# Kernel tuning notes

Measured on AMD Instinct MI355X. Metric: run time of the kernel, lower is better.

Reference implementation:

```python
import jax, jax.numpy as jnp
import numpy as np

MAX_BIN = 256
N_SAMPLES = 2_000_000
N_FEATURES = 64


def setup_inputs() -> dict:
    key = jax.random.key(0)
    k1, k2, k3 = jax.random.split(key, 3)
    X = jax.random.randint(k1, (N_SAMPLES, N_FEATURES), 0, MAX_BIN, dtype=jnp.int32)
    gradient = jax.random.normal(k2, (N_SAMPLES,), dtype=jnp.float32)
    hessian = jax.random.uniform(k3, (N_SAMPLES,), dtype=jnp.float32)
    return {"X": X, "gradient": gradient, "hessian": hessian}


def reference(X, gradient, hessian):
    # PGBM split_decision: Gl[f, b] = sum_i gradient[i] * (X[i, f] <= b)
    # Implemented as a per-feature histogram scatter-add, then cumsum over bins.
    def per_feature(xf):  # xf: [N] int bins for one feature
        hg = jax.ops.segment_sum(gradient, xf, num_segments=MAX_BIN)
        hh = jax.ops.segment_sum(hessian, xf, num_segments=MAX_BIN)
        return hg, hh

    hist_g, hist_h = jax.vmap(per_feature, in_axes=1)(X)  # [F, MAX_BIN] each
    Gl = jnp.cumsum(hist_g, axis=1)  # left gradient sums per (feature, bin)
    Hl = jnp.cumsum(hist_h, axis=1)  # left hessian sums per (feature, bin)
    return Gl[None], Hl[None]  # [1, F, MAX_BIN] each, matching unsqueeze(0)
```

## Files before the change

kernel.cpp:

```cpp
#include <hip/hip_runtime.h>

#define N_FEAT 64
#define NBINS 256
#define NB2 260
#define HIST_FLOATS (N_FEAT * NBINS)
#define NBLOCKS 256
#define BLOCK_T 128
#define CHUNK 32
#define PARTIAL_FLOATS 32768
#define WS_PARTIAL_BYTES ((size_t)NBLOCKS * PARTIAL_FLOATS * sizeof(float))

__device__ __forceinline__ void load_chunk(const int* __restrict__ X,
    const float* __restrict__ grad, const float* __restrict__ hess,
    int c, int rend, int col, int lane, int (&bins)[CHUNK], float& val)
{
    #pragma unroll
    for (int j = 0; j < CHUNK; ++j) {
        int r = c + j; r = r < rend ? r : rend - 1;
        bins[j] = X[(size_t)r * N_FEAT + col];
    }
    int rv = c + (lane & 31); rv = rv < rend ? rv : rend - 1;
    val = (lane < 32) ? grad[rv] : hess[rv];
}

__device__ __forceinline__ void process_chunk(float (&hist)[2][N_FEAT][NB2],
    int w, int lane, int c, int rend, const int (&bins)[CHUNK], float val)
{
    #pragma unroll
    for (int q = 0; q < CHUNK / 4; ++q) {
        float v[4]; int b[4];
        #pragma unroll
        for (int j = 0; j < 4; ++j) {
            const int r = c + q * 4 + j;
            const float vv = __shfl(val, (lane & 32) + q * 4 + j);
            v[j] = (r < rend) ? vv : 0.f;
            b[j] = bins[q * 4 + j];
        }
        const bool e10 = b[1] == b[0];
        const bool e20 = b[2] == b[0], e21 = b[2] == b[1];
        const bool e30 = b[3] == b[0], e31 = b[3] == b[1], e32 = b[3] == b[2];
        const float v0 = v[0] + (e10 ? v[1] : 0.f) + (e20 ? v[2] : 0.f) + (e30 ? v[3] : 0.f);
        const float v1 = v[1] + ((!e20 && e21) ? v[2] : 0.f) + ((!e30 && e31) ? v[3] : 0.f);
        const float v2 = v[2] + ((!e30 && !e31 && e32) ? v[3] : 0.f);
        const float v3 = v[3];
        const int a0 = b[0];
        const int a1 = e10                 ? 256 : b[1];
        const int a2 = (e20 || e21)        ? 257 : b[2];
        const int a3 = (e30 || e31 || e32) ? 258 : b[3];
        const float t0 = hist[w][lane][a0];
        const float t1 = hist[w][lane][a1];
        const float t2 = hist[w][lane][a2];
        const float t3 = hist[w][lane][a3];
        hist[w][lane][a0] = t0 + v0;
        hist[w][lane][a1] = t1 + v1;
        hist[w][lane][a2] = t2 + v2;
        hist[w][lane][a3] = t3 + v3;
    }
}

__global__ __launch_bounds__(BLOCK_T, 1) void _split_hist_kernel(
    const int* __restrict__ X, const float* __restrict__ grad,
    const float* __restrict__ hess, float* __restrict__ ws, int n, int mode)
{
    __shared__ float hist[2][N_FEAT][NB2];
    const int tid  = threadIdx.x;
    const int w    = tid >> 6;
    const int lane = tid & 63;

    for (int i = tid; i < 2 * N_FEAT * NB2; i += BLOCK_T)
        (&hist[0][0][0])[i] = 0.f;
    __syncthreads();

    const int col  = w * 32 + (lane & 31);
    const int R    = (n + NBLOCKS - 1) / NBLOCKS;
    const int rbeg = blockIdx.x * R;
    const int rend = min(rbeg + R, n);

    if (rbeg < rend) {
        int   binsA[CHUNK], binsB[CHUNK];
        float valA, valB;
        load_chunk(X, grad, hess, rbeg, rend, col, lane, binsA, valA);
        for (int c = rbeg; c < rend; c += 2 * CHUNK) {
            const int c1 = c + CHUNK, c2 = c + 2 * CHUNK;
            if (c1 < rend)
                load_chunk(X, grad, hess, c1, rend, col, lane, binsB, valB);
            process_chunk(hist, w, lane, c, rend, binsA, valA);
            if (c1 < rend) {
                if (c2 < rend)
                    load_chunk(X, grad, hess, c2, rend, col, lane, binsA, valA);
                process_chunk(hist, w, lane, c1, rend, binsB, valB);
            }
        }
    }
    __syncthreads();

    if (mode) {
        float* dst = ws + (size_t)blockIdx.x * PARTIAL_FLOATS;
        for (int i = tid; i < PARTIAL_FLOATS; i += BLOCK_T) {
            const int wv  = i >> 14;
            const int reg = (i >> 8) & 63;
            const int bin = i & 255;
            dst[i] = hist[wv][reg][bin];
        }
    } else {
        for (int i = tid; i < PARTIAL_FLOATS; i += BLOCK_T) {
            const int wv   = i >> 14;
            const int reg  = (i >> 8) & 63;
            const int bin  = i & 255;
            const int type = reg >> 5;
            const int feat = wv * 32 + (reg & 31);
            unsafeAtomicAdd(&ws[type * HIST_FLOATS + feat * NBINS + bin],
                            hist[wv][reg][bin]);
        }
    }
}

__global__ __launch_bounds__(NBINS) void _split_scan_kernel(
    const float* __restrict__ ws, float* __restrict__ out, int mode)
{
    __shared__ float s[NBINS];
    const int row = blockIdx.x;
    const int t   = threadIdx.x;

    float acc;
    if (mode) {
        const int type = row >> 6;
        const int feat = row & 63;
        const int wv   = feat >> 5;
        const int reg  = (type << 5) | (feat & 31);
        const size_t slot = ((size_t)wv << 14) | (reg << 8) | t;
        acc = 0.f;
        for (int p = 0; p < NBLOCKS; ++p)
            acc += ws[(size_t)p * PARTIAL_FLOATS + slot];
    } else {
        acc = ws[row * NBINS + t];
    }
    s[t] = acc;
    __syncthreads();

    #pragma unroll
    for (int off = 1; off < NBINS; off <<= 1) {
        float x = (t >= off) ? s[t - off] : 0.f;
        __syncthreads();
        s[t] += x;
        __syncthreads();
    }
    out[row * NBINS + t] = s[t];
}

extern "C" void kernel_launch(void* const* d_in, const int* in_sizes, int n_in,
                              void* d_out, int out_size, void* d_ws, size_t ws_size,
                              hipStream_t stream) {
    const int*   X    = (const int*)d_in[0];
    const float* grad = (const float*)d_in[1];
    const float* hess = (const float*)d_in[2];
    float*       out  = (float*)d_out;
    float*       ws   = (float*)d_ws;
    const int n = in_sizes[1];

    const int mode = (ws_size >= WS_PARTIAL_BYTES) ? 1 : 0;
    if (!mode)
        hipMemsetAsync(d_ws, 0, 2 * HIST_FLOATS * sizeof(float), stream);

    hipLaunchKernelGGL(_split_hist_kernel, dim3(NBLOCKS), dim3(BLOCK_T), 0, stream,
                       X, grad, hess, ws, n, mode);
    hipLaunchKernelGGL(_split_scan_kernel, dim3(2 * N_FEAT), dim3(NBINS), 0, stream,
                       ws, out, mode);
}
```

Baseline: 1.148 ms.

## Assign one wave per value type with one lane per feature, vectorizing value loads

Each wave now handles either gradient or hessian across all 64 features: each lane owns one feature column, and wave 0 reads gradient while wave 1 reads hessian. Previously each wave covered 32 features and split its lanes between the two value types. Values are now loaded per thread as float4 vectors instead of being broadcast with cross-lane shuffles. Each row's X loads are therefore 64 contiguous ints per wave, and both waves read the same X rows, doubling X read traffic through cache. Rows per block are rounded to a multiple of the chunk size so the fast unguarded load path is taken, and the partial-histogram layout now matches the output directly, simplifying the atomic and scan indexing.

After: 942.9 us. 1.22x faster.

```diff
diff --git a/kernel.cpp b/kernel.cpp
--- a/kernel.cpp
+++ b/kernel.cpp
@@ -7,54 +7,64 @@
 #define NBLOCKS 256
 #define BLOCK_T 128
 #define CHUNK 32
-#define PARTIAL_FLOATS 32768
+#define PARTIAL_FLOATS (2 * HIST_FLOATS)
 #define WS_PARTIAL_BYTES ((size_t)NBLOCKS * PARTIAL_FLOATS * sizeof(float))
 
-__device__ __forceinline__ void load_chunk(const int* __restrict__ X,
-    const float* __restrict__ grad, const float* __restrict__ hess,
-    int c, int rend, int col, int lane, int (&bins)[CHUNK], float& val)
+__device__ __forceinline__ void load_bins(const int* __restrict__ Xl,
+    int c, int rend, int (&bins)[CHUNK])
 {
-    #pragma unroll
-    for (int j = 0; j < CHUNK; ++j) {
-        int r = c + j; r = r < rend ? r : rend - 1;
-        bins[j] = X[(size_t)r * N_FEAT + col];
+    if (c + CHUNK <= rend) {
+        #pragma unroll
+        for (int j = 0; j < CHUNK; ++j)
+            bins[j] = Xl[(size_t)(c + j) * N_FEAT];
+    } else {
+        #pragma unroll
+        for (int j = 0; j < CHUNK; ++j) {
+            int r = c + j; r = r < rend ? r : rend - 1;
+            bins[j] = Xl[(size_t)r * N_FEAT];
+        }
     }
-    int rv = c + (lane & 31); rv = rv < rend ? rv : rend - 1;
-    val = (lane < 32) ? grad[rv] : hess[rv];
 }
 
-__device__ __forceinline__ void process_chunk(float (&hist)[2][N_FEAT][NB2],
-    int w, int lane, int c, int rend, const int (&bins)[CHUNK], float val)
+__device__ __forceinline__ void load_vals(const float* __restrict__ vp,
+    int c, int rend, float (&val)[CHUNK])
+{
+    if (c + CHUNK <= rend) {
+        #pragma unroll
+        for (int j = 0; j < CHUNK / 4; ++j) {
+            const float4 v4 = *reinterpret_cast<const float4*>(vp + c + 4 * j);
+            val[4*j+0] = v4.x; val[4*j+1] = v4.y; val[4*j+2] = v4.z; val[4*j+3] = v4.w;
+        }
+    } else {
+        #pragma unroll
+        for (int j = 0; j < CHUNK; ++j)
+            val[j] = (c + j < rend) ? vp[c + j] : 0.f;
+    }
+}
+
+__device__ __forceinline__ void process_chunk(float* __restrict__ hrow,
+    const int (&bins)[CHUNK], const float (&val)[CHUNK])
 {
     #pragma unroll
     for (int q = 0; q < CHUNK / 4; ++q) {
-        float v[4]; int b[4];
-        #pragma unroll
-        for (int j = 0; j < 4; ++j) {
-            const int r = c + q * 4 + j;
-            const float vv = __shfl(val, (lane & 32) + q * 4 + j);
-            v[j] = (r < rend) ? vv : 0.f;
-            b[j] = bins[q * 4 + j];
-        }
-        const bool e10 = b[1] == b[0];
-        const bool e20 = b[2] == b[0], e21 = b[2] == b[1];
-        const bool e30 = b[3] == b[0], e31 = b[3] == b[1], e32 = b[3] == b[2];
-        const float v0 = v[0] + (e10 ? v[1] : 0.f) + (e20 ? v[2] : 0.f) + (e30 ? v[3] : 0.f);
-        const float v1 = v[1] + ((!e20 && e21) ? v[2] : 0.f) + ((!e30 && e31) ? v[3] : 0.f);
-        const float v2 = v[2] + ((!e30 && !e31 && e32) ? v[3] : 0.f);
-        const float v3 = v[3];
-        const int a0 = b[0];
-        const int a1 = e10                 ? 256 : b[1];
-        const int a2 = (e20 || e21)        ? 257 : b[2];
-        const int a3 = (e30 || e31 || e32) ? 258 : b[3];
-        const float t0 = hist[w][lane][a0];
-        const float t1 = hist[w][lane][a1];
-        const float t2 = hist[w][lane][a2];
-        const float t3 = hist[w][lane][a3];
-        hist[w][lane][a0] = t0 + v0;
-        hist[w][lane][a1] = t1 + v1;
-        hist[w][lane][a2] = t2 + v2;
-        hist[w][lane][a3] = t3 + v3;
+        const int   b0 = bins[4*q+0], b1 = bins[4*q+1], b2 = bins[4*q+2], b3 = bins[4*q+3];
+        const float v0 = val[4*q+0], v1 = val[4*q+1], v2 = val[4*q+2], v3 = val[4*q+3];
+        const bool e10 = b1 == b0;
+        const bool e20 = b2 == b0, e21 = b2 == b1;
+        const bool e30 = b3 == b0, e31 = b3 == b1, e32 = b3 == b2;
+        const float s0 = v0 + (e10 ? v1 : 0.f) + (e20 ? v2 : 0.f) + (e30 ? v3 : 0.f);
+        const float s1 = v1 + ((!e20 && e21) ? v2 : 0.f) + ((!e30 && e31) ? v3 : 0.f);
+        const float s2 = v2 + ((!e30 && !e31 && e32) ? v3 : 0.f);
+        const float s3 = v3;
+        const int a0 = b0;
+        const int a1 = e10                 ? 256 : b1;
+        const int a2 = (e20 || e21)        ? 257 : b2;
+        const int a3 = (e30 || e31 || e32) ? 258 : b3;
+        const float t0 = hrow[a0], t1 = hrow[a1], t2 = hrow[a2], t3 = hrow[a3];
+        hrow[a0] = t0 + s0;
+        hrow[a1] = t1 + s1;
+        hrow[a2] = t2 + s2;
+        hrow[a3] = t3 + s3;
     }
 }
 
@@ -71,24 +81,32 @@
         (&hist[0][0][0])[i] = 0.f;
     __syncthreads();
 
-    const int col  = w * 32 + (lane & 31);
-    const int R    = (n + NBLOCKS - 1) / NBLOCKS;
+    const float* vp   = w ? hess : grad;
+    const int*   Xl   = X + lane;
+    float*       hrow = &hist[w][lane][0];
+
+    const int R    = (((n + NBLOCKS - 1) / NBLOCKS) + CHUNK - 1) / CHUNK * CHUNK;
     const int rbeg = blockIdx.x * R;
     const int rend = min(rbeg + R, n);
 
     if (rbeg < rend) {
         int   binsA[CHUNK], binsB[CHUNK];
-        float valA, valB;
-        load_chunk(X, grad, hess, rbeg, rend, col, lane, binsA, valA);
+        float valA[CHUNK], valB[CHUNK];
+        load_bins(Xl, rbeg, rend, binsA);
+        load_vals(vp, rbeg, rend, valA);
         for (int c = rbeg; c < rend; c += 2 * CHUNK) {
             const int c1 = c + CHUNK, c2 = c + 2 * CHUNK;
-            if (c1 < rend)
-                load_chunk(X, grad, hess, c1, rend, col, lane, binsB, valB);
-            process_chunk(hist, w, lane, c, rend, binsA, valA);
             if (c1 < rend) {
-                if (c2 < rend)
-                    load_chunk(X, grad, hess, c2, rend, col, lane, binsA, valA);
-                process_chunk(hist, w, lane, c1, rend, binsB, valB);
+                load_bins(Xl, c1, rend, binsB);
+                load_vals(vp, c1, rend, valB);
+            }
+            process_chunk(hrow, binsA, valA);
+            if (c1 < rend) {
+                if (c2 < rend) {
+                    load_bins(Xl, c2, rend, binsA);
+                    load_vals(vp, c2, rend, valA);
+                }
+                process_chunk(hrow, binsB, valB);
             }
         }
     }
@@ -97,20 +115,17 @@
     if (mode) {
         float* dst = ws + (size_t)blockIdx.x * PARTIAL_FLOATS;
         for (int i = tid; i < PARTIAL_FLOATS; i += BLOCK_T) {
-            const int wv  = i >> 14;
-            const int reg = (i >> 8) & 63;
+            const int ty  = i >> 14;
+            const int fe  = (i >> 8) & 63;
             const int bin = i & 255;
-            dst[i] = hist[wv][reg][bin];
+            dst[i] = hist[ty][fe][bin];
         }
     } else {
         for (int i = tid; i < PARTIAL_FLOATS; i += BLOCK_T) {
-            const int wv   = i >> 14;
-            const int reg  = (i >> 8) & 63;
-            const int bin  = i & 255;
-            const int type = reg >> 5;
-            const int feat = wv * 32 + (reg & 31);
-            unsafeAtomicAdd(&ws[type * HIST_FLOATS + feat * NBINS + bin],
-                            hist[wv][reg][bin]);
+            const int ty  = i >> 14;
+            const int fe  = (i >> 8) & 63;
+            const int bin = i & 255;
+            unsafeAtomicAdd(&ws[i], hist[ty][fe][bin]);
         }
     }
 }
@@ -122,14 +137,9 @@
     const int row = blockIdx.x;
     const int t   = threadIdx.x;
 
-    float acc;
+    float acc = 0.f;
     if (mode) {
-        const int type = row >> 6;
-        const int feat = row & 63;
-        const int wv   = feat >> 5;
-        const int reg  = (type << 5) | (feat & 31);
-        const size_t slot = ((size_t)wv << 14) | (reg << 8) | t;
-        acc = 0.f;
+        const size_t slot = (size_t)row * NBINS + t;
         for (int p = 0; p < NBLOCKS; ++p)
             acc += ws[(size_t)p * PARTIAL_FLOATS + slot];
     } else {
```
